# Kernel tuning notes

Measured on AMD Instinct MI355X. Metric: run time of the kernel, lower is better.

## Reference

```python
import jax, jax.numpy as jnp
import numpy as np

IN_DIM = 128
OUT_DIM = 128
HEADS = 4
HEAD_DIM = OUT_DIM // HEADS
N_NODES = 50000
N_EDGES = 800000
NEG_SLOPE = 0.2
LN_EPS = 1e-5


def setup_inputs() -> dict:
    key = jax.random.key(0)
    ks = jax.random.split(key, 10)
    x = jax.random.normal(ks[0], (N_NODES, IN_DIM), dtype=jnp.float32)
    edge_index = jax.random.randint(ks[1], (2, N_EDGES), 0, N_NODES, dtype=jnp.int64)
    s = 1.0 / np.sqrt(IN_DIM)
    W_l = jax.random.normal(ks[2], (IN_DIM, HEADS * HEAD_DIM), dtype=jnp.float32) * s
    b_l = jnp.zeros((HEADS * HEAD_DIM,), dtype=jnp.float32)
    W_r = jax.random.normal(ks[3], (IN_DIM, HEADS * HEAD_DIM), dtype=jnp.float32) * s
    b_r = jnp.zeros((HEADS * HEAD_DIM,), dtype=jnp.float32)
    att = jax.random.normal(ks[4], (HEADS, HEAD_DIM), dtype=jnp.float32) * (1.0 / np.sqrt(HEAD_DIM))
    bias = jnp.zeros((HEADS * HEAD_DIM,), dtype=jnp.float32)
    gamma = jnp.ones((OUT_DIM,), dtype=jnp.float32)
    beta = jnp.zeros((OUT_DIM,), dtype=jnp.float32)
    return {"x": x, "edge_index": edge_index, "W_l": W_l, "b_l": b_l,
            "W_r": W_r, "b_r": b_r, "att": att, "bias": bias,
            "gamma": gamma, "beta": beta}


def reference(x, edge_index, W_l, b_l, W_r, b_r, att, bias, gamma, beta):
    N = x.shape[0]
    src, dst = edge_index[0], edge_index[1]
    # GATv2: separate linear transforms for source and target nodes
    xl = (x @ W_l + b_l).reshape(N, HEADS, HEAD_DIM)  # source / message features
    xr = (x @ W_r + b_r).reshape(N, HEADS, HEAD_DIM)  # target features
    # per-edge attention logits: a^T . leaky_relu(xl[src] + xr[dst])  -> [E, H]
    h = jax.nn.leaky_relu(xl[src] + xr[dst], NEG_SLOPE)
    e = jnp.einsum('ehd,hd->eh', h, att)
    # segment softmax over edges grouped by destination node
    m = jax.ops.segment_max(e, dst, num_segments=N)
    m = jnp.where(jnp.isfinite(m), m, 0.0)  # guard empty segments
    ex = jnp.exp(e - m[dst])
    denom = jax.ops.segment_sum(ex, dst, num_segments=N)
    alpha = ex / (denom[dst] + 1e-16)  # [E, H]
    # scatter-add weighted source features (dropout omitted: eval mode)
    out = jax.ops.segment_sum(alpha[:, :, None] * xl[src], dst, num_segments=N)
    out = out.reshape(N, HEADS * HEAD_DIM) + bias
    # residual (in_dim == out_dim) + LayerNorm
    out = out + x
    mu = out.mean(axis=-1, keepdims=True)
    var = ((out - mu) ** 2).mean(axis=-1, keepdims=True)
    return (out - mu) * jax.lax.rsqrt(var + LN_EPS) * gamma + beta
```

## Files before the change

### kernel.cpp

```cpp
#include <hip/hip_runtime.h>
#include <math.h>

#define NEG_SLOPE 0.2f
#define LN_EPS 1e-5f
#define CAP 64
#define HB 8192
#define SLOTS 4608
#define XSTR 136
#define SMEM_BYTES (64 * XSTR * 2 + 32768)

typedef __attribute__((ext_vector_type(8))) short s8v;
typedef __attribute__((ext_vector_type(8))) unsigned short u8v;
typedef __attribute__((ext_vector_type(4))) float f4v;

__device__ inline unsigned short f2bf(float f) {
    unsigned u = __float_as_uint(f);
    return (unsigned short)((u + 0x7FFFu + ((u >> 16) & 1u)) >> 16);
}
__device__ inline float bf2f(unsigned short h) {
    return __uint_as_float((unsigned)h << 16);
}

__global__ __launch_bounds__(256) void pre_kernel(
    const float* __restrict__ Wl, const float* __restrict__ Wr,
    unsigned short* __restrict__ packL, unsigned short* __restrict__ packR,
    int* __restrict__ gcur, int NBKT) {
    const int bid = blockIdx.x, tid = threadIdx.x;
    if (bid < 2) {
        const float* W = bid ? Wr : Wl;
        unsigned short* pk = bid ? packR : packL;
        for (int idx = tid; idx < 16384; idx += 256) {
            int j = idx & 7;
            int lane = (idx >> 3) & 63;
            int ntt = idx >> 9;
            int t = ntt & 3, nt = ntt >> 2;
            int k = t * 32 + (lane >> 4) * 8 + j;
            int n = nt * 16 + (lane & 15);
            pk[idx] = f2bf(W[k * 128 + n]);
        }
        return;
    }
    if (tid < NBKT) gcur[tid] = 0;
}

__global__ __launch_bounds__(256) void scat_tf_kernel(
    const int* __restrict__ src, const int* __restrict__ dst,
    int* __restrict__ gcur, unsigned* __restrict__ part,
    const float* __restrict__ x,
    const unsigned short* __restrict__ packL, const unsigned short* __restrict__ packR,
    const float* __restrict__ bl, const float* __restrict__ br,
    unsigned short* __restrict__ xl, float* __restrict__ xr,
    int N, int E, int NBKT, int NSC, int TBS) {
    const int bid = blockIdx.x, tid = threadIdx.x;
    __shared__ __align__(16) char smem[SMEM_BYTES];

    if (bid < NSC) {
        int* cnt  = (int*)smem;
        int* base = (int*)smem + 256;
        for (int t = tid; t < NBKT; t += 256) cnt[t] = 0;
        __syncthreads();
        const int e0 = bid * HB;
        for (int j = tid; j < HB; j += 256) {
            int e = e0 + j;
            if (e < E) atomicAdd(&cnt[dst[e] >> 8], 1);
        }
        __syncthreads();
        for (int t = tid; t < NBKT; t += 256) {
            base[t] = atomicAdd(&gcur[t], cnt[t]);
            cnt[t] = 0;
        }
        __syncthreads();
        for (int j = tid; j < HB; j += 256) {
            int e = e0 + j;
            if (e < E) {
                int d = dst[e];
                int b = d >> 8;
                int r = atomicAdd(&cnt[b], 1);
                int pos = base[b] + r;
                if (pos < SLOTS)
                    part[(size_t)b * SLOTS + pos] = ((unsigned)d << 16) | (unsigned)src[e];
            }
        }
        return;
    }

    const int rb = bid - NSC;
    const int side = (rb >= TBS);
    const int tb = side ? rb - TBS : rb;
    unsigned short* xs = (unsigned short*)smem;
    unsigned short* pks = (unsigned short*)(smem + 64 * XSTR * 2);
    const int blk0 = tb * 64;
    const unsigned short* __restrict__ pk = side ? packR : packL;
    const float* __restrict__ bb = side ? br : bl;

    #pragma unroll
    for (int it = 0; it < 8; ++it) {
        int slot = tid + it * 256;
        int row = slot >> 5, c4 = slot & 31;
        int node = blk0 + row;
        float4 v = make_float4(0.f, 0.f, 0.f, 0.f);
        if (node < N) v = *(const float4*)&x[(size_t)node * 128 + 4 * c4];
        ushort4 o;
        o.x = f2bf(v.x); o.y = f2bf(v.y); o.z = f2bf(v.z); o.w = f2bf(v.w);
        *(ushort4*)&xs[row * XSTR + 4 * c4] = o;
    }
    #pragma unroll
    for (int it = 0; it < 8; ++it) {
        int slot = tid + it * 256;
        *(float4*)&pks[slot * 8] = *(const float4*)&pk[slot * 8];
    }
    __syncthreads();

    const int wv = tid >> 6, lane = tid & 63;
    const int row = lane & 15, q = lane >> 4;
    const int node0 = blk0 + wv * 16;

    s8v afrag[4];
    #pragma unroll
    for (int t = 0; t < 4; ++t)
        afrag[t] = *(const s8v*)&xs[(wv * 16 + row) * XSTR + t * 32 + q * 8];

    f4v acc[8];
    #pragma unroll
    for (int nt = 0; nt < 8; ++nt) acc[nt] = (f4v){0.f, 0.f, 0.f, 0.f};

    #pragma unroll
    for (int t = 0; t < 4; ++t) {
        #pragma unroll
        for (int nt = 0; nt < 8; ++nt) {
            s8v bfr = *(const s8v*)&pks[(((nt * 4 + t) * 64 + lane)) * 8];
            acc[nt] = __builtin_amdgcn_mfma_f32_16x16x32_bf16(afrag[t], bfr, acc[nt], 0, 0, 0);
        }
    }

    #pragma unroll
    for (int nt = 0; nt < 8; ++nt) {
        float bcol = bb[nt * 16 + row];
        #pragma unroll
        for (int r2 = 0; r2 < 4; ++r2) {
            int nd = node0 + q * 4 + r2;
            if (nd < N) {
                float val = acc[nt][r2] + bcol;
                if (side) xr[(size_t)nd * 128 + nt * 16 + row] = val;
                else      xl[(size_t)nd * 128 + nt * 16 + row] = f2bf(val);
            }
        }
    }
}

__global__ __launch_bounds__(1024) void fill_kernel(
    const unsigned* __restrict__ part, const int* __restrict__ gcur,
    unsigned short* __restrict__ csr, int* __restrict__ deg, int N) {
    const int b = blockIdx.x, tid = threadIdx.x;
    __shared__ int cur[256];
    if (tid < 256) cur[tid] = 0;
    __syncthreads();
    int cnt = gcur[b];
    if (cnt > SLOTS) cnt = SLOTS;
    const unsigned* seg = part + (size_t)b * SLOTS;
    for (int i = tid; i < cnt; i += 1024) {
        unsigned rec = seg[i];
        int d = rec >> 16;
        int pos = atomicAdd(&cur[d & 255], 1);
        if (pos < CAP) csr[(size_t)d * CAP + pos] = (unsigned short)(rec & 0xFFFFu);
    }
    __syncthreads();
    int node = b * 256 + tid;
    if (tid < 256 && node < N) deg[node] = cur[tid];
}

__global__ __launch_bounds__(256) void gat_kernel(
    const int* __restrict__ deg_arr, const unsigned short* __restrict__ csr,
    const unsigned short* __restrict__ xl, const float* __restrict__ xr,
    const float* __restrict__ att, const float* __restrict__ x,
    const float* __restrict__ bias, const float* __restrict__ gamma,
    const float* __restrict__ beta, float* __restrict__ out, int N) {
    const int node = blockIdx.x * 4 + (threadIdx.x >> 6);
    const int lane = threadIdx.x & 63;
    if (node >= N) return;
    const int sub = lane & 15;
    const int eg  = lane >> 4;
    const int f0  = sub * 8;

    float xrf[8], av[8];
    {
        float4 a0 = *(const float4*)&xr[(size_t)node * 128 + f0];
        float4 a1 = *(const float4*)&xr[(size_t)node * 128 + f0 + 4];
        xrf[0] = a0.x; xrf[1] = a0.y; xrf[2] = a0.z; xrf[3] = a0.w;
        xrf[4] = a1.x; xrf[5] = a1.y; xrf[6] = a1.z; xrf[7] = a1.w;
        float4 c0 = *(const float4*)&att[f0];
        float4 c1 = *(const float4*)&att[f0 + 4];
        av[0] = c0.x; av[1] = c0.y; av[2] = c0.z; av[3] = c0.w;
        av[4] = c1.x; av[5] = c1.y; av[6] = c1.z; av[7] = c1.w;
    }

    int dg = deg_arr[node]; if (dg > CAP) dg = CAP;
    const unsigned short* crow = csr + (size_t)node * CAP;

    float den = 0.f;
    float acc[8] = {0.f, 0.f, 0.f, 0.f, 0.f, 0.f, 0.f, 0.f};

    u8v buf0 = {0,0,0,0,0,0,0,0}, buf1 = {0,0,0,0,0,0,0,0};
    if (eg < dg)     buf0 = *(const u8v*)&xl[(size_t)crow[eg] * 128 + f0];
    if (eg + 4 < dg) buf1 = *(const u8v*)&xl[(size_t)crow[eg + 4] * 128 + f0];

    for (int i = eg; i < dg; i += 4) {
        u8v cur = buf0;
        buf0 = buf1;
        if (i + 8 < dg) buf1 = *(const u8v*)&xl[(size_t)crow[i + 8] * 128 + f0];

        float xf[8];
        float p = 0.f;
        #pragma unroll
        for (int j = 0; j < 8; ++j) {
            xf[j] = bf2f(cur[j]);
            float t = xf[j] + xrf[j];
            float h = fmaxf(t, t * NEG_SLOPE);
            p = fmaf(h, av[j], p);
        }
        p += __shfl_xor(p, 1);
        p += __shfl_xor(p, 2);
        float w = __expf(p);
        den += w;
        #pragma unroll
        for (int j = 0; j < 8; ++j) acc[j] = fmaf(w, xf[j], acc[j]);
    }

    den += __shfl_xor(den, 16); den += __shfl_xor(den, 32);
    #pragma unroll
    for (int j = 0; j < 8; ++j) {
        acc[j] += __shfl_xor(acc[j], 16);
        acc[j] += __shfl_xor(acc[j], 32);
    }

    const float inv = 1.0f / (den + 1e-16f);
    float v[8];
    {
        float4 b0 = *(const float4*)&bias[f0];
        float4 b1 = *(const float4*)&bias[f0 + 4];
        float4 r0 = *(const float4*)&x[(size_t)node * 128 + f0];
        float4 r1 = *(const float4*)&x[(size_t)node * 128 + f0 + 4];
        const float bbf[8] = {b0.x, b0.y, b0.z, b0.w, b1.x, b1.y, b1.z, b1.w};
        const float rrf[8] = {r0.x, r0.y, r0.z, r0.w, r1.x, r1.y, r1.z, r1.w};
        #pragma unroll
        for (int j = 0; j < 8; ++j) v[j] = acc[j] * inv + bbf[j] + rrf[j];
    }

    float s = v[0] + v[1] + v[2] + v[3] + v[4] + v[5] + v[6] + v[7];
    s += __shfl_xor(s, 1); s += __shfl_xor(s, 2);
    s += __shfl_xor(s, 4); s += __shfl_xor(s, 8);
    const float mu = s * (1.0f / 128.0f);

    float d[8], vs = 0.f;
    #pragma unroll
    for (int j = 0; j < 8; ++j) { d[j] = v[j] - mu; vs = fmaf(d[j], d[j], vs); }
    vs += __shfl_xor(vs, 1); vs += __shfl_xor(vs, 2);
    vs += __shfl_xor(vs, 4); vs += __shfl_xor(vs, 8);
    const float rstd = rsqrtf(vs * (1.0f / 128.0f) + LN_EPS);

    if (eg == 0) {
        float4 g0 = *(const float4*)&gamma[f0];
        float4 g1 = *(const float4*)&gamma[f0 + 4];
        float4 e0 = *(const float4*)&beta[f0];
        float4 e1 = *(const float4*)&beta[f0 + 4];
        float4 o0, o1;
        o0.x = d[0] * rstd * g0.x + e0.x;  o0.y = d[1] * rstd * g0.y + e0.y;
        o0.z = d[2] * rstd * g0.z + e0.z;  o0.w = d[3] * rstd * g0.w + e0.w;
        o1.x = d[4] * rstd * g1.x + e1.x;  o1.y = d[5] * rstd * g1.y + e1.y;
        o1.z = d[6] * rstd * g1.z + e1.z;  o1.w = d[7] * rstd * g1.w + e1.w;
        *(float4*)&out[(size_t)node * 128 + f0]     = o0;
        *(float4*)&out[(size_t)node * 128 + f0 + 4] = o1;
    }
}

extern "C" void kernel_launch(void* const* d_in, const int* in_sizes, int n_in,
                              void* d_out, int out_size, void* d_ws, size_t ws_size,
                              hipStream_t stream) {
    const float* x     = (const float*)d_in[0];
    const int*   ei    = (const int*)d_in[1];
    const float* Wl    = (const float*)d_in[2];
    const float* bl    = (const float*)d_in[3];
    const float* Wr    = (const float*)d_in[4];
    const float* br    = (const float*)d_in[5];
    const float* att   = (const float*)d_in[6];
    const float* bias  = (const float*)d_in[7];
    const float* gamma = (const float*)d_in[8];
    const float* beta  = (const float*)d_in[9];

    const int N = in_sizes[0] / 128;
    const int E = in_sizes[1] / 2;
    const int* src = ei;
    const int* dst = ei + E;

    const int NBKT = (N + 255) >> 8;
    const int NSC  = (E + HB - 1) / HB;
    const int TBS  = (N + 63) / 64;

    char* w = (char*)d_ws;
    unsigned short* xl    = (unsigned short*)w;  w += (size_t)N * 128 * sizeof(unsigned short);
    float*          xr    = (float*)w;           w += (size_t)N * 128 * sizeof(float);
    unsigned short* packL = (unsigned short*)w;  w += 16384 * sizeof(unsigned short);
    unsigned short* packR = (unsigned short*)w;  w += 16384 * sizeof(unsigned short);
    int*            gcur  = (int*)w;             w += 256 * sizeof(int);
    unsigned*       part  = (unsigned*)w;        w += (size_t)NBKT * SLOTS * sizeof(unsigned);
    unsigned short* csr   = (unsigned short*)w;  w += (size_t)N * CAP * sizeof(unsigned short);
    int*            deg   = (int*)w;             w += (size_t)N * sizeof(int);

    pre_kernel<<<3, 256, 0, stream>>>(Wl, Wr, packL, packR, gcur, NBKT);
    scat_tf_kernel<<<NSC + 2 * TBS, 256, 0, stream>>>(
        src, dst, gcur, part, x, packL, packR, bl, br, xl, xr, N, E, NBKT, NSC, TBS);
    fill_kernel<<<NBKT, 1024, 0, stream>>>(part, gcur, csr, deg, N);
    gat_kernel<<<(N + 3) / 4, 256, 0, stream>>>(
        deg, csr, xl, xr, att, x, bias, gamma, beta, (float*)d_out, N);
}
```

Measured before the change: 184.1 us.

## Build CSR directly with global per-node atomics and drop bucket-partition fill pass

Replaces the two-stage bucketed partition (shared-memory histogram, global bucket offsets, separate fill kernel) with direct global atomicAdd on per-node degree counters that write source indices straight into the fixed-capacity CSR. The degree array is now zeroed in pre_kernel. This removes one kernel launch and the round trip through the partition buffer. The cost is about 800k scattered global atomics instead of shared-memory ones. Separately, the transform blocks now read packed weight fragments directly from global memory instead of staging them in LDS, which shrinks shared memory to raise occupancy (launch bounds set to 4 blocks per CU).

```diff
diff --git a/kernel.cpp b/kernel.cpp
--- a/kernel.cpp
+++ b/kernel.cpp
@@ -5,9 +5,7 @@
 #define LN_EPS 1e-5f
 #define CAP 64
 #define HB 8192
-#define SLOTS 4608
 #define XSTR 136
-#define SMEM_BYTES (64 * XSTR * 2 + 32768)
 
 typedef __attribute__((ext_vector_type(8))) short s8v;
 typedef __attribute__((ext_vector_type(8))) unsigned short u8v;
@@ -24,7 +22,7 @@
 __global__ __launch_bounds__(256) void pre_kernel(
     const float* __restrict__ Wl, const float* __restrict__ Wr,
     unsigned short* __restrict__ packL, unsigned short* __restrict__ packR,
-    int* __restrict__ gcur, int NBKT) {
+    int* __restrict__ deg, int N) {
     const int bid = blockIdx.x, tid = threadIdx.x;
     if (bid < 2) {
         const float* W = bid ? Wr : Wl;
@@ -40,55 +38,38 @@
         }
         return;
     }
-    if (tid < NBKT) gcur[tid] = 0;
-}
-
-__global__ __launch_bounds__(256) void scat_tf_kernel(
+    int i = (bid - 2) * 256 + tid;
+    if (i < N) deg[i] = 0;
+}
+
+__global__ __launch_bounds__(256, 4) void scat_tf_kernel(
     const int* __restrict__ src, const int* __restrict__ dst,
-    int* __restrict__ gcur, unsigned* __restrict__ part,
+    int* __restrict__ deg, unsigned short* __restrict__ csr,
     const float* __restrict__ x,
     const unsigned short* __restrict__ packL, const unsigned short* __restrict__ packR,
     const float* __restrict__ bl, const float* __restrict__ br,
     unsigned short* __restrict__ xl, float* __restrict__ xr,
-    int N, int E, int NBKT, int NSC, int TBS) {
+    int N, int E, int NSC, int TBS) {
     const int bid = blockIdx.x, tid = threadIdx.x;
-    __shared__ __align__(16) char smem[SMEM_BYTES];
 
     if (bid < NSC) {
-        int* cnt  = (int*)smem;
-        int* base = (int*)smem + 256;
-        for (int t = tid; t < NBKT; t += 256) cnt[t] = 0;
-        __syncthreads();
         const int e0 = bid * HB;
-        for (int j = tid; j < HB; j += 256) {
-            int e = e0 + j;
-            if (e < E) atomicAdd(&cnt[dst[e] >> 8], 1);
-        }
-        __syncthreads();
-        for (int t = tid; t < NBKT; t += 256) {
-            base[t] = atomicAdd(&gcur[t], cnt[t]);
-            cnt[t] = 0;
-        }
-        __syncthreads();
         for (int j = tid; j < HB; j += 256) {
             int e = e0 + j;
             if (e < E) {
                 int d = dst[e];
-                int b = d >> 8;
-                int r = atomicAdd(&cnt[b], 1);
-                int pos = base[b] + r;
-                if (pos < SLOTS)
-                    part[(size_t)b * SLOTS + pos] = ((unsigned)d << 16) | (unsigned)src[e];
+                int pos = atomicAdd(&deg[d], 1);
+                if (pos < CAP)
+                    csr[(size_t)d * CAP + pos] = (unsigned short)src[e];
             }
         }
         return;
     }
 
+    __shared__ __align__(16) unsigned short xs[64 * XSTR];
     const int rb = bid - NSC;
     const int side = (rb >= TBS);
     const int tb = side ? rb - TBS : rb;
-    unsigned short* xs = (unsigned short*)smem;
-    unsigned short* pks = (unsigned short*)(smem + 64 * XSTR * 2);
     const int blk0 = tb * 64;
     const unsigned short* __restrict__ pk = side ? packR : packL;
     const float* __restrict__ bb = side ? br : bl;
@@ -104,11 +85,6 @@
         o.x = f2bf(v.x); o.y = f2bf(v.y); o.z = f2bf(v.z); o.w = f2bf(v.w);
         *(ushort4*)&xs[row * XSTR + 4 * c4] = o;
     }
-    #pragma unroll
-    for (int it = 0; it < 8; ++it) {
-        int slot = tid + it * 256;
-        *(float4*)&pks[slot * 8] = *(const float4*)&pk[slot * 8];
-    }
     __syncthreads();
 
     const int wv = tid >> 6, lane = tid & 63;
@@ -127,9 +103,15 @@
     #pragma unroll
     for (int t = 0; t < 4; ++t) {
         #pragma unroll
-        for (int nt = 0; nt < 8; ++nt) {
-            s8v bfr = *(const s8v*)&pks[(((nt * 4 + t) * 64 + lane)) * 8];
-            acc[nt] = __builtin_amdgcn_mfma_f32_16x16x32_bf16(afrag[t], bfr, acc[nt], 0, 0, 0);
+        for (int np = 0; np < 2; ++np) {
+            s8v bfr[4];
+            #pragma unroll
+            for (int u = 0; u < 4; ++u)
+                bfr[u] = *(const s8v*)&pk[(((np * 4 + u) * 4 + t) * 64 + lane) * 8];
+            #pragma unroll
+            for (int u = 0; u < 4; ++u)
+                acc[np * 4 + u] = __builtin_amdgcn_mfma_f32_16x16x32_bf16(
+                    afrag[t], bfr[u], acc[np * 4 + u], 0, 0, 0);
         }
     }
 
@@ -146,27 +128,6 @@
             }
         }
     }
-}
-
-__global__ __launch_bounds__(1024) void fill_kernel(
-    const unsigned* __restrict__ part, const int* __restrict__ gcur,
-    unsigned short* __restrict__ csr, int* __restrict__ deg, int N) {
-    const int b = blockIdx.x, tid = threadIdx.x;
-    __shared__ int cur[256];
-    if (tid < 256) cur[tid] = 0;
-    __syncthreads();
-    int cnt = gcur[b];
-    if (cnt > SLOTS) cnt = SLOTS;
-    const unsigned* seg = part + (size_t)b * SLOTS;
-    for (int i = tid; i < cnt; i += 1024) {
-        unsigned rec = seg[i];
-        int d = rec >> 16;
-        int pos = atomicAdd(&cur[d & 255], 1);
-        if (pos < CAP) csr[(size_t)d * CAP + pos] = (unsigned short)(rec & 0xFFFFu);
-    }
-    __syncthreads();
-    int node = b * 256 + tid;
-    if (tid < 256 && node < N) deg[node] = cur[tid];
 }
 
 __global__ __launch_bounds__(256) void gat_kernel(
@@ -292,24 +253,21 @@
     const int* src = ei;
     const int* dst = ei + E;
 
-    const int NBKT = (N + 255) >> 8;
-    const int NSC  = (E + HB - 1) / HB;
-    const int TBS  = (N + 63) / 64;
+    const int NSC = (E + HB - 1) / HB;
+    const int TBS = (N + 63) / 64;
+    const int ZB  = (N + 255) / 256;
 
     char* w = (char*)d_ws;
     unsigned short* xl    = (unsigned short*)w;  w += (size_t)N * 128 * sizeof(unsigned short);
     float*          xr    = (float*)w;           w += (size_t)N * 128 * sizeof(float);
     unsigned short* packL = (unsigned short*)w;  w += 16384 * sizeof(unsigned short);
     unsigned short* packR = (unsigned short*)w;  w += 16384 * sizeof(unsigned short);
-    int*            gcur  = (int*)w;             w += 256 * sizeof(int);
-    unsigned*       part  = (unsigned*)w;        w += (size_t)NBKT * SLOTS * sizeof(unsigned);
     unsigned short* csr   = (unsigned short*)w;  w += (size_t)N * CAP * sizeof(unsigned short);
     int*            deg   = (int*)w;             w += (size_t)N * sizeof(int);
 
-    pre_kernel<<<3, 256, 0, stream>>>(Wl, Wr, packL, packR, gcur, NBKT);
+    pre_kernel<<<2 + ZB, 256, 0, stream>>>(Wl, Wr, packL, packR, deg, N);
     scat_tf_kernel<<<NSC + 2 * TBS, 256, 0, stream>>>(
-        src, dst, gcur, part, x, packL, packR, bl, br, xl, xr, N, E, NBKT, NSC, TBS);
-    fill_kernel<<<NBKT, 1024, 0, stream>>>(part, gcur, csr, deg, N);
+        src, dst, deg, csr, x, packL, packR, bl, br, xl, xr, N, E, NSC, TBS);
     gat_kernel<<<(N + 3) / 4, 256, 0, stream>>>(
         deg, csr, xl, xr, att, x, bias, gamma, beta, (float*)d_out, N);
 }
```

After: 197.9 us. 1.07x slower.
